# Kernel tuning notes

Measured on AMD Instinct MI355X. Metric: run time of the kernel, lower is better.

## Reference

```python
import jax, jax.numpy as jnp
import numpy as np

DIM = 2048
NUM_HEADS = 4  # hardcoded in RetNext.__init__
HEAD_DIM = DIM // NUM_HEADS
B, T = 4, 4096


def setup_inputs() -> dict:
    key = jax.random.key(0)
    ks = jax.random.split(key, 7)
    s = 1.0 / np.sqrt(DIM)  # roughly nn.Linear init scale
    return {
        "x": jax.random.normal(ks[0], (B, T, DIM), dtype=jnp.float32),
        "Wk": jax.random.normal(ks[1], (DIM, DIM), dtype=jnp.float32) * s,
        "bk": jax.random.normal(ks[2], (DIM,), dtype=jnp.float32) * s,
        "Wq": jax.random.normal(ks[3], (DIM, DIM), dtype=jnp.float32) * s,
        "bq": jax.random.normal(ks[4], (DIM,), dtype=jnp.float32) * s,
        "Wv": jax.random.normal(ks[5], (DIM, DIM), dtype=jnp.float32) * s,
        "bv": jax.random.normal(ks[6], (DIM,), dtype=jnp.float32) * s,
    }


def reference(x, Wk, bk, Wq, bq, Wv, bv):
    bsz, seq_len, _ = x.shape
    # nn.Linear: y = x @ W.T + b
    k = x @ Wk.T + bk
    q = x @ Wq.T + bq
    v = x @ Wv.T + bv
    # (b, s, h, d) -> (b, h, s, d)
    k = k.reshape(bsz, seq_len, NUM_HEADS, HEAD_DIM).transpose(0, 2, 1, 3)
    q = q.reshape(bsz, seq_len, NUM_HEADS, HEAD_DIM).transpose(0, 2, 1, 3)
    v = v.reshape(bsz, seq_len, NUM_HEADS, HEAD_DIM).transpose(0, 2, 1, 3)
    # states = k^T @ v : (b, h, d, d)
    states = jnp.einsum("bhsd,bhse->bhde", k, v)
    # out = q @ states : (b, h, s, d) -- returned WITHOUT reshape, as in the source
    out = jnp.einsum("bhsd,bhde->bhse", q, states)
    return out
```

## Files before the change

### kernel.cpp

```cpp
#include <hip/hip_runtime.h>
#include <cstdint>
#include <cstddef>

typedef __bf16 bf16;
typedef bf16 bf16x8 __attribute__((ext_vector_type(8)));
typedef float f32x4 __attribute__((ext_vector_type(4)));
typedef unsigned short u16;
typedef u16 u16x4 __attribute__((ext_vector_type(4)));
typedef u16 u16x8 __attribute__((ext_vector_type(8)));

__device__ __forceinline__ u16 f2bf(float f) {
    uint32_t u = __builtin_bit_cast(uint32_t, f);
    u += 0x7FFFu + ((u >> 16) & 1u);
    return (u16)(u >> 16);
}

#define AS1C(p) ((const __attribute__((address_space(1))) uint32_t*)(p))
#define AS3(p)  ((__attribute__((address_space(3))) uint32_t*)(p))
#define MFMA16  __builtin_amdgcn_mfma_f32_16x16x32_bf16

__device__ __forceinline__ void gemm_core(const bf16* __restrict__ Ablk,
                                          const bf16* __restrict__ Btblk,
                                          int lda, int ldb, int K,
                                          f32x4 acc[4][4])
{
    __shared__ bf16 lA[4096];
    __shared__ bf16 lB[4096];

    const int tid  = threadIdx.x;
    const int wave = tid >> 6;
    const int lane = tid & 63;
    const int lrow = lane >> 2;
    const int kcol = (lane & 3) << 3;

    const bf16* ga0 = Ablk  + (size_t)(wave * 32 + lrow) * lda + kcol;
    const bf16* ga1 = ga0 + (size_t)16 * lda;
    const bf16* gb0 = Btblk + (size_t)(wave * 32 + lrow) * ldb + kcol;
    const bf16* gb1 = gb0 + (size_t)16 * ldb;
    bf16* la0 = &lA[wave * 1024];
    bf16* la1 = &lA[wave * 1024 + 512];
    bf16* lb0 = &lB[wave * 1024];
    bf16* lb1 = &lB[wave * 1024 + 512];

    const int wm    = (wave >> 1) * 64;
    const int wn    = (wave & 1) * 64;
    const int col16 = lane & 15;
    const int quad  = lane >> 4;
    const bf16* pa = &lA[(wm + col16) * 32 + quad * 8];
    const bf16* pb = &lB[(wn + col16) * 32 + quad * 8];

    for (int kb = 0; kb < K; kb += 32) {
        __builtin_amdgcn_global_load_lds(AS1C(ga0 + kb), AS3(la0), 16, 0, 0);
        __builtin_amdgcn_global_load_lds(AS1C(ga1 + kb), AS3(la1), 16, 0, 0);
        __builtin_amdgcn_global_load_lds(AS1C(gb0 + kb), AS3(lb0), 16, 0, 0);
        __builtin_amdgcn_global_load_lds(AS1C(gb1 + kb), AS3(lb1), 16, 0, 0);
        __syncthreads();

        bf16x8 av[4], bv[4];
        #pragma unroll
        for (int i = 0; i < 4; ++i) av[i] = *(const bf16x8*)(pa + i * 512);
        #pragma unroll
        for (int i = 0; i < 4; ++i) bv[i] = *(const bf16x8*)(pb + i * 512);

        #pragma unroll
        for (int mi = 0; mi < 4; ++mi)
            #pragma unroll
            for (int ni = 0; ni < 4; ++ni)
                acc[mi][ni] = MFMA16(av[mi], bv[ni], acc[mi][ni], 0, 0, 0);
        __syncthreads();
    }
}

__global__ __launch_bounds__(256) void cast_bf16(const float* __restrict__ src,
                                                 u16* __restrict__ dst, int n8)
{
    int i = blockIdx.x * 256 + threadIdx.x;
    if (i >= n8) return;
    const float4* s = (const float4*)src + (size_t)i * 2;
    float4 f0 = s[0], f1 = s[1];
    u16x8 o;
    o[0] = f2bf(f0.x); o[1] = f2bf(f0.y); o[2] = f2bf(f0.z); o[3] = f2bf(f0.w);
    o[4] = f2bf(f1.x); o[5] = f2bf(f1.y); o[6] = f2bf(f1.z); o[7] = f2bf(f1.w);
    *((u16x8*)dst + i) = o;
}

__global__ __launch_bounds__(256) void reduce_cast(const float* __restrict__ sp,
                                                   u16* __restrict__ dst, int n4)
{
    int i = blockIdx.x * 256 + threadIdx.x;
    if (i >= n4) return;
    float4 a = ((const float4*)sp)[i];
    float4 b = ((const float4*)(sp + 4194304))[i];
    u16x4 o;
    o[0] = f2bf(a.x + b.x); o[1] = f2bf(a.y + b.y);
    o[2] = f2bf(a.z + b.z); o[3] = f2bf(a.w + b.w);
    ((u16x4*)dst)[i] = o;
}

__global__ __launch_bounds__(512, 2) void gemm_qkv(
    const bf16* __restrict__ xb,
    const bf16* __restrict__ Wkb, const bf16* __restrict__ Wqb, const bf16* __restrict__ Wvb,
    const float* __restrict__ bk, const float* __restrict__ bq, const float* __restrict__ bv,
    u16* __restrict__ qout, u16* __restrict__ kT, u16* __restrict__ vT)
{
    __shared__ bf16 smem[49152];
    char* sm = (char*)smem;

    const int bx = blockIdx.x;
    const int by = blockIdx.y;
    const int region = by >> 3;
    const int nloc = (by & 7) << 8;

    const bf16* W     = (region == 0) ? Wkb : (region == 1) ? Wqb : Wvb;
    const float* bias = (region == 0) ? bk  : (region == 1) ? bq  : bv;

    const bf16* Ablk = xb + (size_t)bx * 256 * 2048;
    const bf16* Bblk = W  + (size_t)nloc * 2048;
    const int lda = 2048, ldb = 2048;
    const int NT = 2048 / 32;

    const int tid  = threadIdx.x;
    const int wave = tid >> 6;
    const int lane = tid & 63;
    const int col16 = lane & 15;
    const int quad  = lane >> 4;
    const int wm = (wave >> 2) * 128;
    const int wn = (wave & 3) * 64;

    const int P0 = tid * 16;
    const int T0 = P0 ^ ((P0 >> 2) & 0x70) ^ ((P0 >> 4) & 0x10);
    const int r0 = T0 >> 6;
    const int ce = (T0 & 63) >> 1;
    const bf16* gA0 = Ablk + (size_t)r0 * lda + ce;
    const bf16* gA1 = Ablk + (size_t)(r0 + 128) * lda + ce;
    const bf16* gB0 = Bblk + (size_t)r0 * ldb + ce;
    const bf16* gB1 = Bblk + (size_t)(r0 + 128) * ldb + ce;
    const int dA0 = wave * 1024;
    const int dA1 = 8192  + wave * 1024;
    const int dB0 = 16384 + wave * 1024;
    const int dB1 = 24576 + wave * 1024;

    int offA[8], offB[4];
    #pragma unroll
    for (int mi = 0; mi < 8; ++mi) {
        int T = (wm + mi * 16 + col16) * 64 + quad * 16;
        offA[mi] = T ^ ((T >> 2) & 0x70);
    }
    #pragma unroll
    for (int ni = 0; ni < 4; ++ni) {
        int T = (wn + ni * 16 + col16) * 64 + quad * 16;
        offB[ni] = 16384 + (T ^ ((T >> 2) & 0x70));
    }

    f32x4 acc[8][4] = {};

#define GLD(src, dst) __builtin_amdgcn_global_load_lds(AS1C(src), AS3(sm + (dst)), 16, 0, 0)

    GLD(gA0,      0 + dA0); GLD(gB0,      0 + dB0);
    GLD(gA1,      0 + dA1); GLD(gB1,      0 + dB1);
    GLD(gA0 + 32, 32768 + dA0); GLD(gB0 + 32, 32768 + dB0);
    GLD(gA1 + 32, 32768 + dA1); GLD(gB1 + 32, 32768 + dB1);
    asm volatile("s_waitcnt vmcnt(4)" ::: "memory");
    __builtin_amdgcn_s_barrier();
    asm volatile("" ::: "memory");

    int buf = 0, sb = 2;
    for (int t = 0; t < NT; ++t) {
        const int  bb  = buf * 32768;
        const int  sbb = sb  * 32768;
        const int  kb  = (t + 2) * 32;
        const bool st  = (t + 2) < NT;

        bf16x8 a0 = *(const bf16x8*)(sm + bb + offA[0]);
        bf16x8 a1 = *(const bf16x8*)(sm + bb + offA[1]);
        bf16x8 a2 = *(const bf16x8*)(sm + bb + offA[2]);
        bf16x8 a3 = *(const bf16x8*)(sm + bb + offA[3]);
        bf16x8 b0 = *(const bf16x8*)(sm + bb + offB[0]);
        bf16x8 b1 = *(const bf16x8*)(sm + bb + offB[1]);
        bf16x8 b2 = *(const bf16x8*)(sm + bb + offB[2]);
        bf16x8 b3 = *(const bf16x8*)(sm + bb + offB[3]);
        if (st) { GLD(gA0 + kb, sbb + dA0); GLD(gB0 + kb, sbb + dB0); }
        asm volatile("" ::: "memory");
        __builtin_amdgcn_s_barrier();
        asm volatile("s_waitcnt lgkmcnt(0)" ::: "memory");
        __builtin_amdgcn_sched_barrier(0);
        __builtin_amdgcn_s_setprio(1);
        acc[0][0] = MFMA16(a0, b0, acc[0][0], 0, 0, 0);
        acc[0][1] = MFMA16(a0, b1, acc[0][1], 0, 0, 0);
        acc[0][2] = MFMA16(a0, b2, acc[0][2], 0, 0, 0);
        acc[0][3] = MFMA16(a0, b3, acc[0][3], 0, 0, 0);
        acc[1][0] = MFMA16(a1, b0, acc[1][0], 0, 0, 0);
        acc[1][1] = MFMA16(a1, b1, acc[1][1], 0, 0, 0);
        acc[1][2] = MFMA16(a1, b2, acc[1][2], 0, 0, 0);
        acc[1][3] = MFMA16(a1, b3, acc[1][3], 0, 0, 0);
        acc[2][0] = MFMA16(a2, b0, acc[2][0], 0, 0, 0);
        acc[2][1] = MFMA16(a2, b1, acc[2][1], 0, 0, 0);
        acc[2][2] = MFMA16(a2, b2, acc[2][2], 0, 0, 0);
        acc[2][3] = MFMA16(a2, b3, acc[2][3], 0, 0, 0);
        acc[3][0] = MFMA16(a3, b0, acc[3][0], 0, 0, 0);
        acc[3][1] = MFMA16(a3, b1, acc[3][1], 0, 0, 0);
        acc[3][2] = MFMA16(a3, b2, acc[3][2], 0, 0, 0);
        acc[3][3] = MFMA16(a3, b3, acc[3][3], 0, 0, 0);
        __builtin_amdgcn_s_setprio(0);
        asm volatile("" ::: "memory");
        __builtin_amdgcn_s_barrier();
        asm volatile("" ::: "memory");

        bf16x8 a4 = *(const bf16x8*)(sm + bb + offA[4]);
        bf16x8 a5 = *(const bf16x8*)(sm + bb + offA[5]);
        bf16x8 a6 = *(const bf16x8*)(sm + bb + offA[6]);
        bf16x8 a7 = *(const bf16x8*)(sm + bb + offA[7]);
        if (st) { GLD(gA1 + kb, sbb + dA1); GLD(gB1 + kb, sbb + dB1); }
        if (st) { asm volatile("s_waitcnt vmcnt(4)" ::: "memory"); }
        else    { asm volatile("s_waitcnt vmcnt(0)" ::: "memory"); }
        asm volatile("" ::: "memory");
        __builtin_amdgcn_s_barrier();
        asm volatile("s_waitcnt lgkmcnt(0)" ::: "memory");
        __builtin_amdgcn_sched_barrier(0);
        __builtin_amdgcn_s_setprio(1);
        acc[4][0] = MFMA16(a4, b0, acc[4][0], 0, 0, 0);
        acc[4][1] = MFMA16(a4, b1, acc[4][1], 0, 0, 0);
        acc[4][2] = MFMA16(a4, b2, acc[4][2], 0, 0, 0);
        acc[4][3] = MFMA16(a4, b3, acc[4][3], 0, 0, 0);
        acc[5][0] = MFMA16(a5, b0, acc[5][0], 0, 0, 0);
        acc[5][1] = MFMA16(a5, b1, acc[5][1], 0, 0, 0);
        acc[5][2] = MFMA16(a5, b2, acc[5][2], 0, 0, 0);
        acc[5][3] = MFMA16(a5, b3, acc[5][3], 0, 0, 0);
        acc[6][0] = MFMA16(a6, b0, acc[6][0], 0, 0, 0);
        acc[6][1] = MFMA16(a6, b1, acc[6][1], 0, 0, 0);
        acc[6][2] = MFMA16(a6, b2, acc[6][2], 0, 0, 0);
        acc[6][3] = MFMA16(a6, b3, acc[6][3], 0, 0, 0);
        acc[7][0] = MFMA16(a7, b0, acc[7][0], 0, 0, 0);
        acc[7][1] = MFMA16(a7, b1, acc[7][1], 0, 0, 0);
        acc[7][2] = MFMA16(a7, b2, acc[7][2], 0, 0, 0);
        acc[7][3] = MFMA16(a7, b3, acc[7][3], 0, 0, 0);
        __builtin_amdgcn_s_setprio(0);
        asm volatile("" ::: "memory");
        __builtin_amdgcn_s_barrier();
        asm volatile("" ::: "memory");

        buf = (buf == 2) ? 0 : buf + 1;
        sb  = (sb  == 2) ? 0 : sb  + 1;
    }
#undef GLD

    if (region == 1) {
        #pragma unroll
        for (int mi = 0; mi < 8; ++mi) {
            int row = bx * 256 + wm + mi * 16 + quad * 4;
            #pragma unroll
            for (int ni = 0; ni < 4; ++ni) {
                int col = nloc + wn + ni * 16 + col16;
                float b = bias[col];
                #pragma unroll
                for (int r = 0; r < 4; ++r)
                    qout[(size_t)(row + r) * 2048 + col] = f2bf(acc[mi][ni][r] + b);
            }
        }
    } else {
        u16* T = (region == 0) ? kT : vT;
        const int b_ = bx >> 4;
        const int h_ = nloc >> 9;
        const int bh = b_ * 4 + h_;
        #pragma unroll
        for (int mi = 0; mi < 8; ++mi) {
            int s = ((bx & 15) * 256) + wm + mi * 16 + quad * 4;
            #pragma unroll
            for (int ni = 0; ni < 4; ++ni) {
                int fcol = nloc + wn + ni * 16 + col16;
                int d = fcol & 511;
                float b = bias[fcol];
                u16x4 p;
                #pragma unroll
                for (int r = 0; r < 4; ++r) p[r] = f2bf(acc[mi][ni][r] + b);
                *(u16x4*)&T[((size_t)(bh * 512 + d)) * 4096 + s] = p;
            }
        }
    }
}

__global__ __launch_bounds__(256) void gemm_states(
    const u16* __restrict__ vT, const u16* __restrict__ kT, float* __restrict__ SP)
{
    const int z  = blockIdx.z;
    const int bh = z >> 1;
    const int kh = z & 1;
    const int m0 = blockIdx.x * 128;
    const int n0 = blockIdx.y * 128;

    f32x4 acc[4][4] = {};
    const size_t base = (size_t)bh * 2097152;
    const size_t koff = (size_t)kh * 2048;
    gemm_core((const bf16*)vT + base + (size_t)m0 * 4096 + koff,
              (const bf16*)kT + base + (size_t)n0 * 4096 + koff,
              4096, 4096, 2048, acc);

    float* P = SP + (size_t)kh * 4194304 + (size_t)bh * 262144;
    const int lane = threadIdx.x & 63, wave = threadIdx.x >> 6;
    const int wm = (wave >> 1) * 64, wn = (wave & 1) * 64;
    const int col16 = lane & 15, quad = lane >> 4;
    #pragma unroll
    for (int mi = 0; mi < 4; ++mi) {
        int row = m0 + wm + mi * 16 + quad * 4;
        #pragma unroll
        for (int ni = 0; ni < 4; ++ni) {
            int col = n0 + wn + ni * 16 + col16;
            #pragma unroll
            for (int r = 0; r < 4; ++r)
                P[(size_t)(row + r) * 512 + col] = acc[mi][ni][r];
        }
    }
}

__global__ __launch_bounds__(256) void gemm_out(
    const u16* __restrict__ qb, const u16* __restrict__ ST, float* __restrict__ out)
{
    const int bh = blockIdx.z;
    const int b_ = bh >> 2, h_ = bh & 3;
    const int m0 = blockIdx.x * 128;
    const int n0 = blockIdx.y * 128;

    f32x4 acc[4][4] = {};
    gemm_core((const bf16*)qb + ((size_t)(b_ * 4096 + m0)) * 2048 + h_ * 512,
              (const bf16*)ST + (size_t)bh * 262144 + (size_t)n0 * 512,
              2048, 512, 512, acc);

    const int lane = threadIdx.x & 63, wave = threadIdx.x >> 6;
    const int wm = (wave >> 1) * 64, wn = (wave & 1) * 64;
    const int col16 = lane & 15, quad = lane >> 4;
    #pragma unroll
    for (int mi = 0; mi < 4; ++mi) {
        int row = m0 + wm + mi * 16 + quad * 4;
        #pragma unroll
        for (int ni = 0; ni < 4; ++ni) {
            int col = n0 + wn + ni * 16 + col16;
            #pragma unroll
            for (int r = 0; r < 4; ++r)
                out[(size_t)bh * 2097152 + (size_t)(row + r) * 512 + col] =
                    acc[mi][ni][r];
        }
    }
}

extern "C" void kernel_launch(void* const* d_in, const int* in_sizes, int n_in,
                              void* d_out, int out_size, void* d_ws, size_t ws_size,
                              hipStream_t stream)
{
    (void)in_sizes; (void)n_in; (void)out_size; (void)ws_size;
    const float* x  = (const float*)d_in[0];
    const float* Wk = (const float*)d_in[1];
    const float* bk = (const float*)d_in[2];
    const float* Wq = (const float*)d_in[3];
    const float* bq = (const float*)d_in[4];
    const float* Wv = (const float*)d_in[5];
    const float* bv = (const float*)d_in[6];
    float* out = (float*)d_out;

    u16* ws  = (u16*)d_ws;
    u16* xb  = ws;
    u16* Wkb = ws  + 33554432;
    u16* Wqb = Wkb + 4194304;
    u16* Wvb = Wqb + 4194304;
    u16* qb  = Wvb + 4194304;
    u16* kT  = qb  + 33554432;
    u16* vT  = kT  + 33554432;
    u16* ST  = vT  + 33554432;
    float* SP = (float*)xb;

    cast_bf16<<<16384, 256, 0, stream>>>(x,  xb,  4194304);
    cast_bf16<<<2048,  256, 0, stream>>>(Wk, Wkb, 524288);
    cast_bf16<<<2048,  256, 0, stream>>>(Wq, Wqb, 524288);
    cast_bf16<<<2048,  256, 0, stream>>>(Wv, Wvb, 524288);

    gemm_qkv<<<dim3(64, 24), 512, 0, stream>>>(
        (const bf16*)xb, (const bf16*)Wkb, (const bf16*)Wqb, (const bf16*)Wvb,
        bk, bq, bv, qb, kT, vT);

    gemm_states<<<dim3(4, 4, 32), 256, 0, stream>>>(vT, kT, SP);
    reduce_cast<<<4096, 256, 0, stream>>>(SP, ST, 1048576);

    gemm_out<<<dim3(32, 4, 16), 256, 0, stream>>>(qb, ST, out);
}
```

Before: 828.3 us.

## Share 256-tile GEMM core, trim barriers, fuse weight casts, deepen states split-K

Moves the 256x256 pipelined GEMM body of gemm_qkv into a reusable gemm256 helper and drops the mid-iteration barrier, lgkmcnt wait and sched_barrier between the LDS reads and the MFMAs. gemm_out now runs on this 512-thread 256x256 tile instead of the 128x128 gemm_core. gemm_states splits K four ways instead of two to launch more blocks, and reduce_cast sums four partial buffers. The three weight casts become a single launch. Fewer barriers lower sync cost but give less control over instruction scheduling, and the deeper split-K adds more partial-sum traffic.

Result: faster. 794.0 us (-4.1%).

```diff
diff --git a/kernel.cpp b/kernel.cpp
--- a/kernel.cpp
+++ b/kernel.cpp
@@ -71,53 +71,13 @@
     }
 }
 
-__global__ __launch_bounds__(256) void cast_bf16(const float* __restrict__ src,
-                                                 u16* __restrict__ dst, int n8)
-{
-    int i = blockIdx.x * 256 + threadIdx.x;
-    if (i >= n8) return;
-    const float4* s = (const float4*)src + (size_t)i * 2;
-    float4 f0 = s[0], f1 = s[1];
-    u16x8 o;
-    o[0] = f2bf(f0.x); o[1] = f2bf(f0.y); o[2] = f2bf(f0.z); o[3] = f2bf(f0.w);
-    o[4] = f2bf(f1.x); o[5] = f2bf(f1.y); o[6] = f2bf(f1.z); o[7] = f2bf(f1.w);
-    *((u16x8*)dst + i) = o;
-}
-
-__global__ __launch_bounds__(256) void reduce_cast(const float* __restrict__ sp,
-                                                   u16* __restrict__ dst, int n4)
-{
-    int i = blockIdx.x * 256 + threadIdx.x;
-    if (i >= n4) return;
-    float4 a = ((const float4*)sp)[i];
-    float4 b = ((const float4*)(sp + 4194304))[i];
-    u16x4 o;
-    o[0] = f2bf(a.x + b.x); o[1] = f2bf(a.y + b.y);
-    o[2] = f2bf(a.z + b.z); o[3] = f2bf(a.w + b.w);
-    ((u16x4*)dst)[i] = o;
-}
-
-__global__ __launch_bounds__(512, 2) void gemm_qkv(
-    const bf16* __restrict__ xb,
-    const bf16* __restrict__ Wkb, const bf16* __restrict__ Wqb, const bf16* __restrict__ Wvb,
-    const float* __restrict__ bk, const float* __restrict__ bq, const float* __restrict__ bv,
-    u16* __restrict__ qout, u16* __restrict__ kT, u16* __restrict__ vT)
+__device__ __forceinline__ void gemm256(const bf16* __restrict__ Ablk,
+                                        const bf16* __restrict__ Btblk,
+                                        int lda, int ldb, int NT,
+                                        f32x4 acc[8][4])
 {
     __shared__ bf16 smem[49152];
     char* sm = (char*)smem;
-
-    const int bx = blockIdx.x;
-    const int by = blockIdx.y;
-    const int region = by >> 3;
-    const int nloc = (by & 7) << 8;
-
-    const bf16* W     = (region == 0) ? Wkb : (region == 1) ? Wqb : Wvb;
-    const float* bias = (region == 0) ? bk  : (region == 1) ? bq  : bv;
-
-    const bf16* Ablk = xb + (size_t)bx * 256 * 2048;
-    const bf16* Bblk = W  + (size_t)nloc * 2048;
-    const int lda = 2048, ldb = 2048;
-    const int NT = 2048 / 32;
 
     const int tid  = threadIdx.x;
     const int wave = tid >> 6;
@@ -133,8 +93,8 @@
     const int ce = (T0 & 63) >> 1;
     const bf16* gA0 = Ablk + (size_t)r0 * lda + ce;
     const bf16* gA1 = Ablk + (size_t)(r0 + 128) * lda + ce;
-    const bf16* gB0 = Bblk + (size_t)r0 * ldb + ce;
-    const bf16* gB1 = Bblk + (size_t)(r0 + 128) * ldb + ce;
+    const bf16* gB0 = Btblk + (size_t)r0 * ldb + ce;
+    const bf16* gB1 = Btblk + (size_t)(r0 + 128) * ldb + ce;
     const int dA0 = wave * 1024;
     const int dA1 = 8192  + wave * 1024;
     const int dB0 = 16384 + wave * 1024;
@@ -151,8 +111,6 @@
         int T = (wn + ni * 16 + col16) * 64 + quad * 16;
         offB[ni] = 16384 + (T ^ ((T >> 2) & 0x70));
     }
-
-    f32x4 acc[8][4] = {};
 
 #define GLD(src, dst) __builtin_amdgcn_global_load_lds(AS1C(src), AS3(sm + (dst)), 16, 0, 0)
 
@@ -180,10 +138,6 @@
         bf16x8 b2 = *(const bf16x8*)(sm + bb + offB[2]);
         bf16x8 b3 = *(const bf16x8*)(sm + bb + offB[3]);
         if (st) { GLD(gA0 + kb, sbb + dA0); GLD(gB0 + kb, sbb + dB0); }
-        asm volatile("" ::: "memory");
-        __builtin_amdgcn_s_barrier();
-        asm volatile("s_waitcnt lgkmcnt(0)" ::: "memory");
-        __builtin_amdgcn_sched_barrier(0);
         __builtin_amdgcn_s_setprio(1);
         acc[0][0] = MFMA16(a0, b0, acc[0][0], 0, 0, 0);
         acc[0][1] = MFMA16(a0, b1, acc[0][1], 0, 0, 0);
@@ -202,7 +156,6 @@
         acc[3][2] = MFMA16(a3, b2, acc[3][2], 0, 0, 0);
         acc[3][3] = MFMA16(a3, b3, acc[3][3], 0, 0, 0);
         __builtin_amdgcn_s_setprio(0);
-        asm volatile("" ::: "memory");
         __builtin_amdgcn_s_barrier();
         asm volatile("" ::: "memory");
 
@@ -213,10 +166,6 @@
         if (st) { GLD(gA1 + kb, sbb + dA1); GLD(gB1 + kb, sbb + dB1); }
         if (st) { asm volatile("s_waitcnt vmcnt(4)" ::: "memory"); }
         else    { asm volatile("s_waitcnt vmcnt(0)" ::: "memory"); }
-        asm volatile("" ::: "memory");
-        __builtin_amdgcn_s_barrier();
-        asm volatile("s_waitcnt lgkmcnt(0)" ::: "memory");
-        __builtin_amdgcn_sched_barrier(0);
         __builtin_amdgcn_s_setprio(1);
         acc[4][0] = MFMA16(a4, b0, acc[4][0], 0, 0, 0);
         acc[4][1] = MFMA16(a4, b1, acc[4][1], 0, 0, 0);
@@ -235,7 +184,6 @@
         acc[7][2] = MFMA16(a7, b2, acc[7][2], 0, 0, 0);
         acc[7][3] = MFMA16(a7, b3, acc[7][3], 0, 0, 0);
         __builtin_amdgcn_s_setprio(0);
-        asm volatile("" ::: "memory");
         __builtin_amdgcn_s_barrier();
         asm volatile("" ::: "memory");
 
@@ -243,6 +191,76 @@
         sb  = (sb  == 2) ? 0 : sb  + 1;
     }
 #undef GLD
+}
+
+__global__ __launch_bounds__(256) void cast_bf16(const float* __restrict__ src,
+                                                 u16* __restrict__ dst, int n8)
+{
+    int i = blockIdx.x * 256 + threadIdx.x;
+    if (i >= n8) return;
+    const float4* s = (const float4*)src + (size_t)i * 2;
+    float4 f0 = s[0], f1 = s[1];
+    u16x8 o;
+    o[0] = f2bf(f0.x); o[1] = f2bf(f0.y); o[2] = f2bf(f0.z); o[3] = f2bf(f0.w);
+    o[4] = f2bf(f1.x); o[5] = f2bf(f1.y); o[6] = f2bf(f1.z); o[7] = f2bf(f1.w);
+    *((u16x8*)dst + i) = o;
+}
+
+__global__ __launch_bounds__(256) void cast_w(const float* __restrict__ Wk,
+                                              const float* __restrict__ Wq,
+                                              const float* __restrict__ Wv,
+                                              u16* __restrict__ dst)
+{
+    const int bx = blockIdx.x;
+    const int region = bx >> 11;
+    const int i = ((bx & 2047) << 8) + threadIdx.x;
+    const float* src = (region == 0) ? Wk : (region == 1) ? Wq : Wv;
+    const float4* s = (const float4*)src + (size_t)i * 2;
+    float4 f0 = s[0], f1 = s[1];
+    u16x8 o;
+    o[0] = f2bf(f0.x); o[1] = f2bf(f0.y); o[2] = f2bf(f0.z); o[3] = f2bf(f0.w);
+    o[4] = f2bf(f1.x); o[5] = f2bf(f1.y); o[6] = f2bf(f1.z); o[7] = f2bf(f1.w);
+    *((u16x8*)dst + (size_t)region * 524288 + i) = o;
+}
+
+__global__ __launch_bounds__(256) void reduce_cast(const float* __restrict__ sp,
+                                                   u16* __restrict__ dst, int n4)
+{
+    int i = blockIdx.x * 256 + threadIdx.x;
+    if (i >= n4) return;
+    float4 a = ((const float4*)sp)[i];
+    float4 b = ((const float4*)(sp + 4194304))[i];
+    float4 c = ((const float4*)(sp + 8388608))[i];
+    float4 d = ((const float4*)(sp + 12582912))[i];
+    u16x4 o;
+    o[0] = f2bf((a.x + b.x) + (c.x + d.x));
+    o[1] = f2bf((a.y + b.y) + (c.y + d.y));
+    o[2] = f2bf((a.z + b.z) + (c.z + d.z));
+    o[3] = f2bf((a.w + b.w) + (c.w + d.w));
+    ((u16x4*)dst)[i] = o;
+}
+
+__global__ __launch_bounds__(512, 2) void gemm_qkv(
+    const bf16* __restrict__ xb,
+    const bf16* __restrict__ Wkb, const bf16* __restrict__ Wqb, const bf16* __restrict__ Wvb,
+    const float* __restrict__ bk, const float* __restrict__ bq, const float* __restrict__ bv,
+    u16* __restrict__ qout, u16* __restrict__ kT, u16* __restrict__ vT)
+{
+    const int bx = blockIdx.x;
+    const int by = blockIdx.y;
+    const int region = by >> 3;
+    const int nloc = (by & 7) << 8;
+
+    const bf16* W     = (region == 0) ? Wkb : (region == 1) ? Wqb : Wvb;
+    const float* bias = (region == 0) ? bk  : (region == 1) ? bq  : bv;
+
+    f32x4 acc[8][4] = {};
+    gemm256(xb + (size_t)bx * 256 * 2048, W + (size_t)nloc * 2048,
+            2048, 2048, 64, acc);
+
+    const int lane = threadIdx.x & 63, wave = threadIdx.x >> 6;
+    const int wm = (wave >> 2) * 128, wn = (wave & 3) * 64;
+    const int col16 = lane & 15, quad = lane >> 4;
 
     if (region == 1) {
         #pragma unroll
@@ -283,17 +301,17 @@
     const u16* __restrict__ vT, const u16* __restrict__ kT, float* __restrict__ SP)
 {
     const int z  = blockIdx.z;
-    const int bh = z >> 1;
-    const int kh = z & 1;
+    const int bh = z >> 2;
+    const int kh = z & 3;
     const int m0 = blockIdx.x * 128;
     const int n0 = blockIdx.y * 128;
 
     f32x4 acc[4][4] = {};
     const size_t base = (size_t)bh * 2097152;
-    const size_t koff = (size_t)kh * 2048;
+    const size_t koff = (size_t)kh * 1024;
     gemm_core((const bf16*)vT + base + (size_t)m0 * 4096 + koff,
               (const bf16*)kT + base + (size_t)n0 * 4096 + koff,
-              4096, 4096, 2048, acc);
+              4096, 4096, 1024, acc);
 
     float* P = SP + (size_t)kh * 4194304 + (size_t)bh * 262144;
     const int lane = threadIdx.x & 63, wave = threadIdx.x >> 6;
@@ -312,24 +330,24 @@
     }
 }
 
-__global__ __launch_bounds__(256) void gemm_out(
+__global__ __launch_bounds__(512, 2) void gemm_out(
     const u16* __restrict__ qb, const u16* __restrict__ ST, float* __restrict__ out)
 {
     const int bh = blockIdx.z;
     const int b_ = bh >> 2, h_ = bh & 3;
-    const int m0 = blockIdx.x * 128;
-    const int n0 = blockIdx.y * 128;
-
-    f32x4 acc[4][4] = {};
-    gemm_core((const bf16*)qb + ((size_t)(b_ * 4096 + m0)) * 2048 + h_ * 512,
-              (const bf16*)ST + (size_t)bh * 262144 + (size_t)n0 * 512,
-              2048, 512, 512, acc);
+    const int m0 = blockIdx.x * 256;
+    const int n0 = blockIdx.y * 256;
+
+    f32x4 acc[8][4] = {};
+    gemm256((const bf16*)qb + ((size_t)(b_ * 4096 + m0)) * 2048 + h_ * 512,
+            (const bf16*)ST + (size_t)bh * 262144 + (size_t)n0 * 512,
+            2048, 512, 16, acc);
 
     const int lane = threadIdx.x & 63, wave = threadIdx.x >> 6;
-    const int wm = (wave >> 1) * 64, wn = (wave & 1) * 64;
+    const int wm = (wave >> 2) * 128, wn = (wave & 3) * 64;
     const int col16 = lane & 15, quad = lane >> 4;
     #pragma unroll
-    for (int mi = 0; mi < 4; ++mi) {
+    for (int mi = 0; mi < 8; ++mi) {
         int row = m0 + wm + mi * 16 + quad * 4;
         #pragma unroll
         for (int ni = 0; ni < 4; ++ni) {
@@ -367,17 +385,15 @@
     u16* ST  = vT  + 33554432;
     float* SP = (float*)xb;
 
-    cast_bf16<<<16384, 256, 0, stream>>>(x,  xb,  4194304);
-    cast_bf16<<<2048,  256, 0, stream>>>(Wk, Wkb, 524288);
-    cast_bf16<<<2048,  256, 0, stream>>>(Wq, Wqb, 524288);
-    cast_bf16<<<2048,  256, 0, stream>>>(Wv, Wvb, 524288);
+    cast_bf16<<<16384, 256, 0, stream>>>(x, xb, 4194304);
+    cast_w<<<6144, 256, 0, stream>>>(Wk, Wq, Wv, Wkb);
 
     gemm_qkv<<<dim3(64, 24), 512, 0, stream>>>(
         (const bf16*)xb, (const bf16*)Wkb, (const bf16*)Wqb, (const bf16*)Wvb,
         bk, bq, bv, qb, kT, vT);
 
-    gemm_states<<<dim3(4, 4, 32), 256, 0, stream>>>(vT, kT, SP);
+    gemm_states<<<dim3(4, 4, 64), 256, 0, stream>>>(vT, kT, SP);
     reduce_cast<<<4096, 256, 0, stream>>>(SP, ST, 1048576);
 
-    gemm_out<<<dim3(32, 4, 16), 256, 0, stream>>>(qb, ST, out);
-}
+    gemm_out<<<dim3(16, 2, 16), 512, 0, stream>>>(qb, ST, out);
+}
```
